# Kernel tuning notes

Measured on AMD Instinct MI355X. Metric: run time of the kernel, lower is better.

## Reference

```python
import jax, jax.numpy as jnp
import numpy as np

T, NC, NQ = 16, 32, 32
H, W, C = 128, 128, 1
DW, DR, DZ = 256, 256, 128
LABEL_DIM, Y_DIM = 2, 2
NHEADS = 8
NFEAT = int(DW * np.log(DW))  # performer default nb_features = int(d*ln d) = 1419


def setup_inputs() -> dict:
    key = jax.random.key(0)
    ks = iter(jax.random.split(key, 48))
    def nrm(shape, scale=0.02):
        return jax.random.normal(next(ks), shape, dtype=jnp.float32) * scale
    z = lambda *s: jnp.zeros(s, jnp.float32)
    return {
        'batch_train_images': jax.random.normal(next(ks), (T, NC, C, H, W), jnp.float32),
        'label_train': jax.random.normal(next(ks), (T, NC, LABEL_DIM), jnp.float32),
        'batch_test_images': jax.random.normal(next(ks), (T, NQ, C, H, W), jnp.float32),
        'conv1_w': nrm((32, C, 3, 3), 0.1), 'conv1_b': z(32),
        'conv2_w': nrm((48, 32, 3, 3), 0.05), 'conv2_b': z(48),
        'conv3_w': nrm((64, 48, 3, 3), 0.05), 'conv3_b': z(64),
        'enc_lw': nrm((DW, 4096)), 'enc_lb': z(DW),
        'ty_w': nrm((DW // 4, LABEL_DIM)), 'ty_b': z(DW // 4),
        'er_w1': nrm((DR, DW + DW // 4), 0.05), 'er_b1': z(DR),
        'er_w2': nrm((DR, DR), 0.05), 'er_b2': z(DR),
        'er_w3': nrm((DR, DR), 0.05), 'er_b3': z(DR),
        'wq': nrm((NHEADS, DW, DW), 0.05), 'wq_b': z(NHEADS, DW),
        'wk': nrm((NHEADS, DW, DW), 0.05), 'wk_b': z(NHEADS, DW),
        'wv': nrm((NHEADS, DW, DW), 0.05), 'wv_b': z(NHEADS, DW),
        'wo_w': nrm((DW, NHEADS * DW), 0.02), 'wo_b': z(DW),
        'rz_w': nrm((DZ, DR), 0.05), 'rz_b': z(DZ),
        'd0_w1': nrm((100, DW + DZ), 0.05), 'd0_b1': z(100),
        'd0_w2': nrm((100, 100), 0.05), 'd0_b2': z(100),
        'd0_w3': nrm((Y_DIM, 100), 0.05), 'd0_b3': z(Y_DIM),
        'proj': jax.random.normal(next(ks), (NFEAT, DW), jnp.float32),
    }


def _conv(x, w, b, stride):
    y = jax.lax.conv_general_dilated(x, w, (stride, stride), [(1, 1), (1, 1)],
                                     dimension_numbers=('NCHW', 'OIHW', 'NCHW'))
    return y + b[None, :, None, None]


def _maxpool2(x):
    return jax.lax.reduce_window(x, -jnp.inf, jax.lax.max, (1, 1, 2, 2), (1, 1, 2, 2), 'VALID')


def _encode(x, c1w, c1b, c2w, c2b, c3w, c3b, lw, lb):
    # BBBEncoder (mean weights): 128->64->32->pool16->8, 64ch, flatten 4096 -> DW
    x = jax.nn.relu(_conv(x, c1w, c1b, 2))
    x = jax.nn.relu(_conv(x, c2w, c2b, 2))
    x = _maxpool2(x)
    x = jax.nn.relu(_conv(x, c3w, c3b, 2))
    x = x.reshape(x.shape[0], -1)  # [B, 4096], NCHW order matches torch view
    return x @ lw.T + lb


def _softmax_kernel(x, proj, is_query):
    # performer softmax-kernel random features
    dn = x.shape[-1] ** -0.25
    ratio = proj.shape[0] ** -0.5
    xn = x * dn
    xd = jnp.einsum('bhnd,fd->bhnf', xn, proj)
    diag = 0.5 * jnp.sum(xn * xn, axis=-1, keepdims=True)
    if is_query:
        m = jnp.max(xd, axis=-1, keepdims=True)
    else:
        m = jnp.max(xd, axis=(-1, -2), keepdims=True)
    return ratio * (jnp.exp(xd - diag - jax.lax.stop_gradient(m)) + 1e-4)


def _forward(batch_train_images, label_train, batch_test_images,
             conv1_w, conv1_b, conv2_w, conv2_b, conv3_w, conv3_b, enc_lw, enc_lb,
             ty_w, ty_b, er_w1, er_b1, er_w2, er_b2, er_w3, er_b3,
             wq, wq_b, wk, wk_b, wv, wv_b, wo_w, wo_b, rz_w, rz_b,
             d0_w1, d0_b1, d0_w2, d0_b2, d0_w3, d0_b3, proj):
    enc = lambda im: _encode(im, conv1_w, conv1_b, conv2_w, conv2_b, conv3_w, conv3_b, enc_lw, enc_lb)
    x_qry = enc(batch_test_images.reshape(-1, C, H, W)).reshape(T, NQ, DW)
    x_ctx = enc(batch_train_images.reshape(-1, C, H, W)).reshape(T, NC, DW)
    ly = label_train @ ty_w.T + ty_b
    x = jnp.concatenate([x_ctx, ly], axis=2)  # [T, NC, DW + DW//4]
    h = jax.nn.relu(x @ er_w1.T + er_b1)
    h = jax.nn.relu(h @ er_w2.T + er_b2)
    rs = h @ er_w3.T + er_b3  # [T, NC, DR]
    # per-head projections (batched over the 8 heads)
    k_all = jnp.einsum('bnd,hed->bhne', x_ctx, wk) + wk_b[None, :, None, :]
    v_all = jnp.einsum('bnd,hed->bhne', rs, wv) + wv_b[None, :, None, :]
    q_all = jnp.einsum('bnd,hed->bhne', x_qry, wq) + wq_b[None, :, None, :]
    qp = _softmax_kernel(q_all, proj, True)   # [T, H, NQ, F]
    kp = _softmax_kernel(k_all, proj, False)  # [T, H, NC, F]
    d_inv = 1.0 / jnp.einsum('bhnf,bhf->bhn', qp, kp.sum(axis=2))
    ctx_mat = jnp.einsum('bhnf,bhne->bhfe', kp, v_all)
    outs = jnp.einsum('bhnf,bhfe->bhne', qp, ctx_mat) * d_inv[..., None]
    outs = outs.transpose(0, 2, 3, 1).reshape(T, NQ, -1)  # permute(0,2,3,1).view
    rep = outs @ wo_w.T + wo_b
    zz = rep @ rz_w.T + rz_b  # [T, NQ, DZ]
    xz = jnp.concatenate([x_qry, zz], axis=-1)
    h = jax.nn.relu(xz @ d0_w1.T + d0_b1)
    h = jax.nn.relu(h @ d0_w2.T + d0_b2)
    return jnp.tanh(h @ d0_w3.T + d0_b3)  # pr_y_mu [T, NQ, Y_DIM]


def reference(batch_train_images, label_train, batch_test_images,
              conv1_w, conv1_b, conv2_w, conv2_b, conv3_w, conv3_b, enc_lw, enc_lb,
              ty_w, ty_b, er_w1, er_b1, er_w2, er_b2, er_w3, er_b3,
              wq, wq_b, wk, wk_b, wv, wv_b, wo_w, wo_b, rz_w, rz_b,
              d0_w1, d0_b1, d0_w2, d0_b2, d0_w3, d0_b3, proj):
    pr_y_mu = _forward(batch_train_images, label_train, batch_test_images,
                       conv1_w, conv1_b, conv2_w, conv2_b, conv3_w, conv3_b, enc_lw, enc_lb,
                       ty_w, ty_b, er_w1, er_b1, er_w2, er_b2, er_w3, er_b3,
                       wq, wq_b, wk, wk_b, wv, wv_b, wo_w, wo_b, rz_w, rz_b,
                       d0_w1, d0_b1, d0_w2, d0_b2, d0_w3, d0_b3, proj)
    kl = jnp.float32(0.0)  # deterministic (mean-weight) BBB encoder -> KL constant
    return (pr_y_mu, kl)
```

## Files before the change

### kernel.cpp

```cpp
#include <hip/hip_runtime.h>
#include <math.h>

#define F_FEAT 1419
static constexpr float DN    = 0.25f;

typedef short short8 __attribute__((ext_vector_type(8)));
typedef float f32x4  __attribute__((ext_vector_type(4)));

static constexpr long OFF_XDQ  = 0;
static constexpr long OFF_XDK  = 5812224;
static constexpr long U_WQH = 0;
static constexpr long U_WQL = 524288;
static constexpr long U_WKH = 1048576;
static constexpr long U_WKL = 1572864;
static constexpr long U_WVH = 2097152;
static constexpr long U_WVL = 2621440;
static constexpr long OFF_ENCT = 4000000;
static constexpr long OFF_REPT = 8400000;
static constexpr long OFF_PA   = 11624448;
static constexpr long U_PH  = 23248896;
static constexpr long U_PL  = 23642112;
static constexpr long U_XCH = 24035328;
static constexpr long U_XCL = 24297472;
static constexpr long U_RSH = 24559616;
static constexpr long U_RSL = 24690688;
static constexpr long U_C3H = 25165824;
static constexpr long U_C3L = 29360128;
static constexpr long U_WOH = 25165824;
static constexpr long U_WOL = 25690112;
static constexpr long BASE     = 16777216;
static constexpr long OFF_XCTX = BASE + 0;
static constexpr long OFF_XQRY = BASE + 131072;
static constexpr long OFF_XCAT = BASE + 262144;
static constexpr long OFF_H1   = BASE + 425984;
static constexpr long OFF_H2   = BASE + 557056;
static constexpr long OFF_RS   = BASE + 688128;
static constexpr long U_QH  = (BASE + 819200) * 2;
static constexpr long U_QL  = U_QH + 1048576;
static constexpr long U_KH  = (BASE + 1867776) * 2;
static constexpr long U_KL  = U_KH + 1048576;
static constexpr long OFF_VA   = BASE + 2916352;
static constexpr long OFF_AW1  = BASE + 3964928;
static constexpr long U_ELH = (BASE + 3977344) * 2;
static constexpr long U_ELL = U_ELH + 1048576;
static constexpr long U_REPH = U_ELH;
static constexpr long U_REPL = U_ELL;
static constexpr long OFF_REP  = BASE + 5025920;
static constexpr long OFF_XZ   = BASE + 5156992;
static constexpr long OFF_DH1  = BASE + 5353600;
static constexpr long OFF_DH2  = BASE + 5404800;
static constexpr long OFF_MD   = BASE + 5456000;
static constexpr long OFF_AW   = 22233216;
static constexpr long OFF_AW3  = 22240128;

__device__ inline unsigned short f2bf(float f) {
    unsigned int x = __float_as_uint(f);
    unsigned int r = x + 0x7fffu + ((x >> 16) & 1u);
    return (unsigned short)(r >> 16);
}
__device__ inline float bf2f(unsigned short h) {
    return __uint_as_float((unsigned int)h << 16);
}
__device__ inline unsigned int cvtpk(float a, float b) {
    unsigned int r;
    asm("v_cvt_pk_bf16_f32 %0, %1, %2" : "=v"(r) : "v"(a), "v"(b));
    return r;
}
__device__ inline unsigned encf(float f) {
    unsigned u = __float_as_uint(f);
    return (u & 0x80000000u) ? ~u : (u | 0x80000000u);
}
__device__ inline float decf(unsigned u) {
    return __uint_as_float((u & 0x80000000u) ? (u & 0x7fffffffu) : ~u);
}

static constexpr int NA1 = 13824;
static constexpr int NA2 = NA1 + 1024;
static constexpr int NA3 = NA2 + 73728;
static constexpr int NA4 = NA3 + 1048576;

__global__ void k_wprepA(const float* __restrict__ w2, const float* __restrict__ w1,
                         const float* __restrict__ w3, const float* __restrict__ elw,
                         unsigned short* __restrict__ Aw, unsigned short* __restrict__ Aw1,
                         unsigned short* __restrict__ Aw3,
                         unsigned short* __restrict__ ELh, unsigned short* __restrict__ ELl)
{
    int i = blockIdx.x * 256 + threadIdx.x;
    if (i < NA1) {
        int ic  = i & 31;
        int m16 = (i >> 5) & 15;
        int emt = i >> 9;
        int mt  = emt % 3, e = emt / 3;
        Aw[i] = f2bf(w2[((mt * 16 + m16) * 32 + ic) * 9 + e]);
    } else if (i < NA2) {
        int j = i - NA1;
        int k = j & 31, m = (j >> 5) & 15, mt = j >> 9;
        Aw1[j] = (k < 9) ? f2bf(w1[(mt * 16 + m) * 9 + k]) : (unsigned short)0;
    } else if (i < NA3) {
        int j = i - NA2;
        int k  = j & 63;
        int m  = (j >> 6) & 15;
        int hl = (j >> 10) & 1;
        int mt = (j >> 11) & 3;
        int e  = j >> 13;
        unsigned short v = 0;
        if (k < 48) {
            float w = w3[((mt * 16 + m) * 48 + k) * 9 + e];
            unsigned short hi = f2bf(w);
            v = hl == 0 ? hi : f2bf(w - bf2f(hi));
        }
        Aw3[j] = v;
    } else if (i < NA4) {
        int j = i - NA3;
        float v = elw[j];
        unsigned short h = f2bf(v);
        ELh[j] = h; ELl[j] = f2bf(v - bf2f(h));
    }
}

static constexpr int NB1 = 393216;
static constexpr int NB2 = NB1 + 1572864;

__global__ void k_wprepB(const float* __restrict__ proj,
                         const float* __restrict__ wq, const float* __restrict__ wk,
                         const float* __restrict__ wv,
                         unsigned short* __restrict__ Ph, unsigned short* __restrict__ Pl,
                         unsigned short* __restrict__ Wqkv)
{
    int i = blockIdx.x * 256 + threadIdx.x;
    if (i < NB1) {
        float v = (i < 363264) ? proj[i] : 0.f;
        unsigned short h = f2bf(v);
        Ph[i] = h; Pl[i] = f2bf(v - bf2f(h));
    } else if (i < NB2) {
        int j = i - NB1;
        int y = j / 524288, jj = j % 524288;
        const float* s = (y == 0) ? wq : (y == 1) ? wk : wv;
        float v = s[jj];
        unsigned short h = f2bf(v);
        Wqkv[(long)y * 1048576 + jj] = h;
        Wqkv[(long)y * 1048576 + 524288 + jj] = f2bf(v - bf2f(h));
    }
}

#define TP 136
__launch_bounds__(256)
__global__ void k_conv12m(const float* __restrict__ train, const float* __restrict__ test,
                          const float* __restrict__ b1,
                          const unsigned short* __restrict__ Aw,
                          const unsigned short* __restrict__ Aw1,
                          const float* __restrict__ b2,
                          unsigned short* __restrict__ pool_out)
{
    const int g   = blockIdx.x;
    const int img = blockIdx.y;
    const float* in = (img < 512) ? (train + (long)img * 16384)
                                  : (test  + (long)(img - 512) * 16384);

    __shared__ unsigned short ring[9 * 66 * 40];
    __shared__ unsigned short tile[19 * TP];

    const int t = threadIdx.x;

    for (int i = t; i < 9 * 40; i += 256) {
        int sl = i / 40, icp = i % 40;
        ring[(sl * 66 + 0) * 40 + icp] = 0;
    }
    if (g == 0)
        for (int i = t; i < 66 * 40; i += 256) ring[i] = 0;
    if (t < 19) *(unsigned int*)&tile[t * TP + 2] = 0u;

    {
        const float4 z4 = make_float4(0.f, 0.f, 0.f, 0.f);
        for (int u = t; u < 19 * 32; u += 256) {
            int row = u >> 5, k = u & 31;
            int r2 = 16 * g - 3 + row;
            float4 v = (r2 >= 0) ? *(const float4*)(in + r2 * 128 + k * 4) : z4;
            uint2 d;
            d.x = cvtpk(v.x, v.y);
            d.y = cvtpk(v.z, v.w);
            *(uint2*)&tile[row * TP + 4 + k * 4] = d;
        }
    }
    __syncthreads();

    const int w    = t >> 6;
    const int lane = t & 63;
    const int cn   = lane & 15;
    const int quad = lane >> 4;

    short8 a1f0 = *(const short8*)&Aw1[(0 * 16 + cn) * 32 + quad * 8];
    short8 a1f1 = *(const short8*)&Aw1[(16 + cn) * 32 + quad * 8];
    float4 bsa = *(const float4*)&b1[quad * 4];
    float4 bsb = *(const float4*)&b1[16 + quad * 4];

    const int px2 = w * 16 + cn;
    const int tb  = 2 * px2 + 2;
    auto do_slice = [&](int sl) {
        const int rb = 2 * sl * TP + tb;
        uint4 pk = make_uint4(0u, 0u, 0u, 0u);
        if (quad == 0) {
            unsigned int w00 = *(const unsigned int*)&tile[rb];
            unsigned int w10 = *(const unsigned int*)&tile[rb + 2];
            unsigned int w01 = *(const unsigned int*)&tile[rb + TP];
            unsigned int w11 = *(const unsigned int*)&tile[rb + TP + 2];
            unsigned int w02 = *(const unsigned int*)&tile[rb + 2 * TP];
            unsigned int w12 = *(const unsigned int*)&tile[rb + 2 * TP + 2];
            pk.x = (w00 >> 16) | (w10 << 16);
            pk.y = (w10 >> 16) | (w01 & 0xffff0000u);
            pk.z = w11;
            pk.w = (w02 >> 16) | (w12 << 16);
        } else if (quad == 1) {
            pk.x = (*(const unsigned int*)&tile[rb + 2 * TP + 2]) >> 16;
        }
        short8 bfr = *(const short8*)&pk;
        f32x4 z = (f32x4){0.f, 0.f, 0.f, 0.f};
        f32x4 c0 = __builtin_amdgcn_mfma_f32_16x16x32_bf16(a1f0, bfr, z, 0, 0, 0);
        f32x4 c1 = __builtin_amdgcn_mfma_f32_16x16x32_bf16(a1f1, bfr, z, 0, 0, 0);
        uint2 u0, u1;
        u0.x = cvtpk(fmaxf(c0[0] + bsa.x, 0.f), fmaxf(c0[1] + bsa.y, 0.f));
        u0.y = cvtpk(fmaxf(c0[2] + bsa.z, 0.f), fmaxf(c0[3] + bsa.w, 0.f));
        u1.x = cvtpk(fmaxf(c1[0] + bsb.x, 0.f), fmaxf(c1[1] + bsb.y, 0.f));
        u1.y = cvtpk(fmaxf(c1[2] + bsb.z, 0.f), fmaxf(c1[3] + bsb.w, 0.f));
        *(uint2*)&ring[(sl * 66 + px2 + 1) * 40 + quad * 4]      = u0;
        *(uint2*)&ring[(sl * 66 + px2 + 1) * 40 + 16 + quad * 4] = u1;
    };
    if (g > 0) do_slice(0);
    #pragma unroll
    for (int sl = 1; sl < 9; sl++) do_slice(sl);

    short8 ca0 = *(const short8*)&Aw[((0 * 3 + 0) * 16 + cn) * 32 + quad * 8];
    short8 ca1 = *(const short8*)&Aw[((0 * 3 + 1) * 16 + cn) * 32 + quad * 8];
    short8 ca2 = *(const short8*)&Aw[((0 * 3 + 2) * 16 + cn) * 32 + quad * 8];
    __syncthreads();

    const int pr = w >> 1, xh = w & 1;
    f32x4 acc[3][2];
    #pragma unroll
    for (int mt = 0; mt < 3; mt++) {
        acc[mt][0] = (f32x4){0.f, 0.f, 0.f, 0.f};
        acc[mt][1] = (f32x4){0.f, 0.f, 0.f, 0.f};
    }

    #pragma unroll
    for (int e = 0; e < 9; e++) {
        int dy = e / 3, dx = e - 3 * dy;
        int c  = 2 * (xh * 16 + cn) + dx;
        int s0 = 4 * pr + dy;
        short8 b0  = *(const short8*)&ring[(s0 * 66 + c) * 40 + quad * 8];
        short8 b1f = *(const short8*)&ring[((s0 + 2) * 66 + c) * 40 + quad * 8];
        short8 na0, na1, na2;
        if (e < 8) {
            na0 = *(const short8*)&Aw[(((e + 1) * 3 + 0) * 16 + cn) * 32 + quad * 8];
            na1 = *(const short8*)&Aw[(((e + 1) * 3 + 1) * 16 + cn) * 32 + quad * 8];
            na2 = *(const short8*)&Aw[(((e + 1) * 3 + 2) * 16 + cn) * 32 + quad * 8];
        }
        acc[0][0] = __builtin_amdgcn_mfma_f32_16x16x32_bf16(ca0, b0,  acc[0][0], 0, 0, 0);
        acc[1][0] = __builtin_amdgcn_mfma_f32_16x16x32_bf16(ca1, b0,  acc[1][0], 0, 0, 0);
        acc[2][0] = __builtin_amdgcn_mfma_f32_16x16x32_bf16(ca2, b0,  acc[2][0], 0, 0, 0);
        acc[0][1] = __builtin_amdgcn_mfma_f32_16x16x32_bf16(ca0, b1f, acc[0][1], 0, 0, 0);
        acc[1][1] = __builtin_amdgcn_mfma_f32_16x16x32_bf16(ca1, b1f, acc[1][1], 0, 0, 0);
        acc[2][1] = __builtin_amdgcn_mfma_f32_16x16x32_bf16(ca2, b1f, acc[2][1], 0, 0, 0);
        if (e < 8) { ca0 = na0; ca1 = na1; ca2 = na2; }
    }

    {
        const int prow = 2 * g + pr;
        const int ppx  = xh * 8 + (cn >> 1);
        unsigned short* pb = pool_out + ((long)img * 256 + prow * 16 + ppx) * 96
                           + ((cn & 1) ? 48 : 0);
        #pragma unroll
        for (int mt = 0; mt < 3; mt++) {
            float4 bv = *(const float4*)&b2[mt * 16 + quad * 4];
            float m0, m1, m2, m3;
            {
                float v;
                v = fmaxf(fmaxf(acc[mt][0][0] + bv.x, acc[mt][1][0] + bv.x), 0.f);
                m0 = fmaxf(v, __shfl_xor(v, 1));
                v = fmaxf(fmaxf(acc[mt][0][1] + bv.y, acc[mt][1][1] + bv.y), 0.f);
                m1 = fmaxf(v, __shfl_xor(v, 1));
                v = fmaxf(fmaxf(acc[mt][0][2] + bv.z, acc[mt][1][2] + bv.z), 0.f);
                m2 = fmaxf(v, __shfl_xor(v, 1));
                v = fmaxf(fmaxf(acc[mt][0][3] + bv.w, acc[mt][1][3] + bv.w), 0.f);
                m3 = fmaxf(v, __shfl_xor(v, 1));
            }
            uint2 hv;
            hv.x = cvtpk(m0, m1);
            hv.y = cvtpk(m2, m3);
            uint2 sv = hv;
            if (cn & 1) {
                float d0 = m0 - bf2f((unsigned short)(hv.x & 0xffffu));
                float d1 = m1 - bf2f((unsigned short)(hv.x >> 16));
                float d2 = m2 - bf2f((unsigned short)(hv.y & 0xffffu));
                float d3 = m3 - bf2f((unsigned short)(hv.y >> 16));
                sv.x = cvtpk(d0, d1);
                sv.y = cvtpk(d2, d3);
            }
            *(uint2*)&pb[mt * 16 + quad * 4] = sv;
        }
    }
}

#define C3PITCH 104
__launch_bounds__(512)
__global__ void k_conv3m(const unsigned short* __restrict__ pool,
                         const unsigned short* __restrict__ Aw3,
                         const float* __restrict__ b3,
                         unsigned short* __restrict__ C3h, unsigned short* __restrict__ C3l)
{
    const int img = blockIdx.x;
    __shared__ unsigned short s_in[30120];
    const int t = threadIdx.x;

    uint4* s4 = (uint4*)s_in;
    const uint4 zz = make_uint4(0, 0, 0, 0);
    for (int i = t; i < 3765; i += 512) s4[i] = zz;
    __syncthreads();
    {
        int p = t >> 1, half = t & 1;
        const uint4* src = (const uint4*)(pool + ((long)img * 256 + p) * 96 + half * 48);
        int r = p >> 4, c = p & 15;
        uint4* dst = (uint4*)(s_in + ((r + 1) * 17 + (c + 1)) * C3PITCH + half * 48);
        #pragma unroll
        for (int j = 0; j < 6; j++) dst[j] = src[j];
    }
    __syncthreads();

    const int w = t >> 6, lane = t & 63;
    const int n = lane & 15, quad = lane >> 4;
    const int mt = w >> 1, ntb = (w & 1) * 2;

    f32x4 acc[2];
    acc[0] = (f32x4){0.f, 0.f, 0.f, 0.f};
    acc[1] = (f32x4){0.f, 0.f, 0.f, 0.f};

    for (int e = 0; e < 9; e++) {
        int dy = e / 3, dx = e - 3 * dy;
        const unsigned short* A0 = Aw3 + (long)(((e * 4 + mt) * 2 + 0) * 16 + n) * 64 + quad * 8;
        const unsigned short* A1 = Aw3 + (long)(((e * 4 + mt) * 2 + 1) * 16 + n) * 64 + quad * 8;
        short8 ah0 = *(const short8*)(A0);
        short8 ah1 = *(const short8*)(A0 + 32);
        short8 al0 = *(const short8*)(A1);
        short8 al1 = *(const short8*)(A1 + 32);
        #pragma unroll
        for (int j = 0; j < 2; j++) {
            int p = (ntb + j) * 16 + n;
            int y = p >> 3, x = p & 7;
            const unsigned short* Bp = s_in + ((2 * y + dy) * 17 + (2 * x + dx)) * C3PITCH + quad * 8;
            short8 bh0 = *(const short8*)(Bp);
            short8 bh1 = *(const short8*)(Bp + 32);
            short8 bl0 = *(const short8*)(Bp + 48);
            short8 bl1 = *(const short8*)(Bp + 48 + 32);
            acc[j] = __builtin_amdgcn_mfma_f32_16x16x32_bf16(ah0, bh0, acc[j], 0, 0, 0);
// ... 92 lines not shown
                    (Yf + (long)z * sY)[(long)row * ldY + col] = v;
                } else if (OUTMODE == 0) {
                    if (B) v += B[col];
                    (Yf + (long)z * sY)[(long)row * ldY + col] = v;
                } else {
                    if (B) v += B[col];
                    unsigned short h = f2bf(v);
                    (Yh + (long)z * sY)[(long)row * ldY + col] = h;
                    (Yl + (long)z * sY)[(long)row * ldY + col] = f2bf(v - bf2f(h));
                }
            }
        }
    }
}

__launch_bounds__(256)
__global__ void mgemm128(const unsigned short* __restrict__ Xh0, const unsigned short* __restrict__ Xl0,
                         const unsigned short* __restrict__ Wh, const unsigned short* __restrict__ Wl,
                         float* __restrict__ Yf, int M, int N, int K, int ldY, float scale,
                         long sX, long sY,
                         unsigned* __restrict__ mqe, unsigned* __restrict__ mke)
{
    const int z = blockIdx.z;
    const unsigned short* Xh = Xh0 + (long)z * sX;
    const unsigned short* Xl = Xl0 + (long)z * sX;

    __shared__ unsigned short sAh[128 * 40], sAl[128 * 40], sBh[128 * 40], sBl[128 * 40];

    const int t = threadIdx.x;
    const int m0 = blockIdx.y * 128, n0 = blockIdx.x * 128;
    const int r = t >> 1, kq = (t & 1) * 16;

    const int w = t >> 6, lane = t & 63;
    const int wm = (w & 1) * 64, wn = (w >> 1) * 64;
    const int cn = lane & 15, quad = lane >> 4;

    f32x4 acc[4][4];
    #pragma unroll
    for (int i = 0; i < 4; i++)
        #pragma unroll
        for (int j = 0; j < 4; j++) acc[i][j] = (f32x4){0.f, 0.f, 0.f, 0.f};

    for (int kb = 0; kb < K; kb += 32) {
        *(uint4*)&sAh[r * 40 + kq]     = *(const uint4*)&Xh[(long)(m0 + r) * K + kb + kq];
        *(uint4*)&sAh[r * 40 + kq + 8] = *(const uint4*)&Xh[(long)(m0 + r) * K + kb + kq + 8];
        *(uint4*)&sAl[r * 40 + kq]     = *(const uint4*)&Xl[(long)(m0 + r) * K + kb + kq];
        *(uint4*)&sAl[r * 40 + kq + 8] = *(const uint4*)&Xl[(long)(m0 + r) * K + kb + kq + 8];
        *(uint4*)&sBh[r * 40 + kq]     = *(const uint4*)&Wh[(long)(n0 + r) * K + kb + kq];
        *(uint4*)&sBh[r * 40 + kq + 8] = *(const uint4*)&Wh[(long)(n0 + r) * K + kb + kq + 8];
        *(uint4*)&sBl[r * 40 + kq]     = *(const uint4*)&Wl[(long)(n0 + r) * K + kb + kq];
        *(uint4*)&sBl[r * 40 + kq + 8] = *(const uint4*)&Wl[(long)(n0 + r) * K + kb + kq + 8];
        __syncthreads();
        short8 axh[4], axl[4], bxh[4], bxl[4];
        #pragma unroll
        for (int i = 0; i < 4; i++) {
            axh[i] = *(const short8*)&sAh[(wm + i * 16 + cn) * 40 + quad * 8];
            axl[i] = *(const short8*)&sAl[(wm + i * 16 + cn) * 40 + quad * 8];
            bxh[i] = *(const short8*)&sBh[(wn + i * 16 + cn) * 40 + quad * 8];
            bxl[i] = *(const short8*)&sBl[(wn + i * 16 + cn) * 40 + quad * 8];
        }
        #pragma unroll
        for (int i = 0; i < 4; i++)
            #pragma unroll
            for (int j = 0; j < 4; j++) {
                acc[i][j] = __builtin_amdgcn_mfma_f32_16x16x32_bf16(axh[i], bxh[j], acc[i][j], 0, 0, 0);
                acc[i][j] = __builtin_amdgcn_mfma_f32_16x16x32_bf16(axh[i], bxl[j], acc[i][j], 0, 0, 0);
                acc[i][j] = __builtin_amdgcn_mfma_f32_16x16x32_bf16(axl[i], bxh[j], acc[i][j], 0, 0, 0);
            }
        __syncthreads();
    }

    float gmax0 = -3e38f, gmax1 = -3e38f;
    #pragma unroll
    for (int i = 0; i < 4; i++) {
        #pragma unroll
        for (int reg = 0; reg < 4; reg++) {
            int row = m0 + wm + i * 16 + quad * 4 + reg;
            float rmax = -3e38f;
            #pragma unroll
            for (int j = 0; j < 4; j++) {
                int col = n0 + wn + j * 16 + cn;
                if (col >= N) continue;
                float v = acc[i][j][reg] * scale;
                (Yf + (long)z * sY)[(long)row * ldY + col] = v;
                rmax = fmaxf(rmax, v);
            }
            if (z == 0) {
                rmax = fmaxf(rmax, __shfl_xor(rmax, 1));
                rmax = fmaxf(rmax, __shfl_xor(rmax, 2));
                rmax = fmaxf(rmax, __shfl_xor(rmax, 4));
                rmax = fmaxf(rmax, __shfl_xor(rmax, 8));
                if (cn == 0) atomicMax(&mqe[row], encf(rmax));
            } else {
                if (i < 2) gmax0 = fmaxf(gmax0, rmax);
                else       gmax1 = fmaxf(gmax1, rmax);
            }
        }
    }
    if (z == 1) {
        for (int d = 1; d < 64; d <<= 1) {
            gmax0 = fmaxf(gmax0, __shfl_xor(gmax0, d));
            gmax1 = fmaxf(gmax1, __shfl_xor(gmax1, d));
        }
        if (lane == 0) {
            atomicMax(&mke[(m0 + wm) >> 5],       encf(gmax0));
            atomicMax(&mke[((m0 + wm) >> 5) + 1], encf(gmax1));
        }
    }
}

__launch_bounds__(256)
__global__ void mgemm128s(const unsigned short* __restrict__ Xh, const unsigned short* __restrict__ Xl,
                          const unsigned short* __restrict__ Wh, const unsigned short* __restrict__ Wl,
                          float* __restrict__ Yf, int M, int N, int K, int ldY,
                          long sY, int kChunk)
{
    const int z = blockIdx.z;
    const int k0 = z * kChunk, k1 = min(K, k0 + kChunk);

    __shared__ unsigned short sAh[128 * 40], sAl[128 * 40], sBh[128 * 40], sBl[128 * 40];

    const int t = threadIdx.x;
    const int m0 = blockIdx.y * 128, n0 = blockIdx.x * 128;
    const int r = t >> 1, kq = (t & 1) * 16;

    const int w = t >> 6, lane = t & 63;
    const int wm = (w & 1) * 64, wn = (w >> 1) * 64;
    const int cn = lane & 15, quad = lane >> 4;

    f32x4 acc[4][4];
    #pragma unroll
    for (int i = 0; i < 4; i++)
        #pragma unroll
        for (int j = 0; j < 4; j++) acc[i][j] = (f32x4){0.f, 0.f, 0.f, 0.f};

    for (int kb = k0; kb < k1; kb += 32) {
        *(uint4*)&sAh[r * 40 + kq]     = *(const uint4*)&Xh[(long)(m0 + r) * K + kb + kq];
        *(uint4*)&sAh[r * 40 + kq + 8] = *(const uint4*)&Xh[(long)(m0 + r) * K + kb + kq + 8];
        *(uint4*)&sAl[r * 40 + kq]     = *(const uint4*)&Xl[(long)(m0 + r) * K + kb + kq];
        *(uint4*)&sAl[r * 40 + kq + 8] = *(const uint4*)&Xl[(long)(m0 + r) * K + kb + kq + 8];
        *(uint4*)&sBh[r * 40 + kq]     = *(const uint4*)&Wh[(long)(n0 + r) * K + kb + kq];
        *(uint4*)&sBh[r * 40 + kq + 8] = *(const uint4*)&Wh[(long)(n0 + r) * K + kb + kq + 8];
        *(uint4*)&sBl[r * 40 + kq]     = *(const uint4*)&Wl[(long)(n0 + r) * K + kb + kq];
        *(uint4*)&sBl[r * 40 + kq + 8] = *(const uint4*)&Wl[(long)(n0 + r) * K + kb + kq + 8];
        __syncthreads();
        short8 axh[4], axl[4], bxh[4], bxl[4];
        #pragma unroll
        for (int i = 0; i < 4; i++) {
            axh[i] = *(const short8*)&sAh[(wm + i * 16 + cn) * 40 + quad * 8];
            axl[i] = *(const short8*)&sAl[(wm + i * 16 + cn) * 40 + quad * 8];
            bxh[i] = *(const short8*)&sBh[(wn + i * 16 + cn) * 40 + quad * 8];
            bxl[i] = *(const short8*)&sBl[(wn + i * 16 + cn) * 40 + quad * 8];
        }
        #pragma unroll
        for (int i = 0; i < 4; i++)
            #pragma unroll
            for (int j = 0; j < 4; j++) {
                acc[i][j] = __builtin_amdgcn_mfma_f32_16x16x32_bf16(axh[i], bxh[j], acc[i][j], 0, 0, 0);
                acc[i][j] = __builtin_amdgcn_mfma_f32_16x16x32_bf16(axh[i], bxl[j], acc[i][j], 0, 0, 0);
                acc[i][j] = __builtin_amdgcn_mfma_f32_16x16x32_bf16(axl[i], bxh[j], acc[i][j], 0, 0, 0);
            }
        __syncthreads();
    }

    float* Y = Yf + (long)z * sY;
    #pragma unroll
    for (int i = 0; i < 4; i++) {
        #pragma unroll
        for (int reg = 0; reg < 4; reg++) {
            int row = m0 + wm + i * 16 + quad * 4 + reg;
            #pragma unroll
            for (int j = 0; j < 4; j++) {
                int col = n0 + wn + j * 16 + cn;
                if (col >= N) continue;
                Y[(long)row * ldY + col] = acc[i][j][reg];
            }
        }
    }
}

__launch_bounds__(256)
__global__ void k_qkv(const unsigned short* __restrict__ XCh, const unsigned short* __restrict__ XCl,
                      const unsigned short* __restrict__ RSh, const unsigned short* __restrict__ RSl,
                      const unsigned short* __restrict__ Wqkv,
                      const float* __restrict__ wqb, const float* __restrict__ wkb,
                      const float* __restrict__ wvb,
                      unsigned short* __restrict__ Qh, unsigned short* __restrict__ Ql,
                      unsigned short* __restrict__ Kh, unsigned short* __restrict__ Kl,
                      float* __restrict__ v_all, float* __restrict__ dq, float* __restrict__ dk)
{
    const int z = blockIdx.z, y = z >> 3, zh = z & 7;
    const unsigned short* Xh = (y == 0) ? XCh + 512 * 256 : (y == 1) ? XCh : RSh;
    const unsigned short* Xl = (y == 0) ? XCl + 512 * 256 : (y == 1) ? XCl : RSl;
    const unsigned short* Wh = Wqkv + (long)y * 1048576 + (long)zh * 65536;
    const unsigned short* Wl = Wh + 524288;
    const float* B = ((y == 0) ? wqb : (y == 1) ? wkb : wvb) + zh * 256;

    __shared__ unsigned short sAh[64 * 40], sAl[64 * 40], sBh[64 * 40], sBl[64 * 40];

    const int t = threadIdx.x;
    const int m0 = blockIdx.y * 64, n0 = blockIdx.x * 64;
    const int r = t >> 2, kq = (t & 3) * 8;
    const int w = t >> 6, lane = t & 63;
    const int wm = (w & 1) * 32, wn = (w >> 1) * 32;
    const int cn = lane & 15, quad = lane >> 4;

    f32x4 acc[2][2];
    acc[0][0] = acc[0][1] = acc[1][0] = acc[1][1] = (f32x4){0.f, 0.f, 0.f, 0.f};

    for (int kb = 0; kb < 256; kb += 32) {
        *(uint4*)&sAh[r * 40 + kq] = *(const uint4*)&Xh[(long)(m0 + r) * 256 + kb + kq];
        *(uint4*)&sAl[r * 40 + kq] = *(const uint4*)&Xl[(long)(m0 + r) * 256 + kb + kq];
        *(uint4*)&sBh[r * 40 + kq] = *(const uint4*)&Wh[(long)(n0 + r) * 256 + kb + kq];
        *(uint4*)&sBl[r * 40 + kq] = *(const uint4*)&Wl[(long)(n0 + r) * 256 + kb + kq];
        __syncthreads();
        short8 axh[2], axl[2], bxh[2], bxl[2];
        #pragma unroll
        for (int i = 0; i < 2; i++) {
            axh[i] = *(const short8*)&sAh[(wm + i * 16 + cn) * 40 + quad * 8];
            axl[i] = *(const short8*)&sAl[(wm + i * 16 + cn) * 40 + quad * 8];
            bxh[i] = *(const short8*)&sBh[(wn + i * 16 + cn) * 40 + quad * 8];
            bxl[i] = *(const short8*)&sBl[(wn + i * 16 + cn) * 40 + quad * 8];
        }
        #pragma unroll
        for (int i = 0; i < 2; i++)
            #pragma unroll
            for (int j = 0; j < 2; j++) {
                acc[i][j] = __builtin_amdgcn_mfma_f32_16x16x32_bf16(axh[i], bxh[j], acc[i][j], 0, 0, 0);
                acc[i][j] = __builtin_amdgcn_mfma_f32_16x16x32_bf16(axh[i], bxl[j], acc[i][j], 0, 0, 0);
                acc[i][j] = __builtin_amdgcn_mfma_f32_16x16x32_bf16(axl[i], bxh[j], acc[i][j], 0, 0, 0);
            }
        __syncthreads();
    }

    unsigned short* Yh = ((y == 0) ? Qh : Kh) + (long)zh * 131072;
    unsigned short* Yl = ((y == 0) ? Ql : Kl) + (long)zh * 131072;
    float* Yf = v_all + (long)zh * 131072;
    float* dacc = ((y == 0) ? dq : dk) + zh * 512;

    #pragma unroll
    for (int i = 0; i < 2; i++) {
        #pragma unroll
        for (int reg = 0; reg < 4; reg++) {
            int row = m0 + wm + i * 16 + quad * 4 + reg;
            float s = 0.f;
            #pragma unroll
            for (int j = 0; j < 2; j++) {
                int col = n0 + wn + j * 16 + cn;
                float v = acc[i][j][reg] + B[col];
                if (y == 2) {
                    Yf[(long)row * 256 + col] = v;
                } else {
                    unsigned short h = f2bf(v);
                    Yh[(long)row * 256 + col] = h;
                    Yl[(long)row * 256 + col] = f2bf(v - bf2f(h));
                    s += v * v;
                }
            }
            if (y < 2) {
                s += __shfl_xor(s, 1); s += __shfl_xor(s, 2);
                s += __shfl_xor(s, 4); s += __shfl_xor(s, 8);
                if (cn == 0) atomicAdd(&dacc[row], s * (1.f / 32.f));
            }
        }
    }
}

__global__ void k_red_enc(const float* __restrict__ tmp, const float* __restrict__ elb,
                          float* __restrict__ x_ctx, unsigned short* __restrict__ XCh,
                          unsigned short* __restrict__ XCl, float* __restrict__ xcat,
                          const float* __restrict__ label, const float* __restrict__ tyw,
                          const float* __restrict__ tyb,
                          const float* __restrict__ wow, unsigned short* __restrict__ WOh,
                          unsigned short* __restrict__ WOl, unsigned* __restrict__ md)
{
    int b = blockIdx.x;
    int tt = threadIdx.x;
    if (b < 1024) {
        int i = b * 256 + tt;
        int r = i >> 8, c = i & 255;
        float v = elb[c];
        #pragma unroll
        for (int z = 0; z < 16; z++) v += tmp[(long)z * 262144 + i];
        x_ctx[i] = v;
        unsigned short h = f2bf(v);
        XCh[i] = h; XCl[i] = f2bf(v - bf2f(h));
        if (r < 512) xcat[r * 320 + c] = v;
    } else if (b < 1152) {
        int i = (b - 1024) * 256 + tt;
        int r = i >> 6, e = i & 63;
        xcat[r * 320 + 256 + e] = tyb[e] + label[r * 2] * tyw[e * 2] + label[r * 2 + 1] * tyw[e * 2 + 1];
    } else if (b < 3200) {
        int i = (b - 1152) * 256 + tt;
        float v = wow[i];
        unsigned short h = f2bf(v);
        WOh[i] = h; WOl[i] = f2bf(v - bf2f(h));
    } else {
        int i = (b - 3200) * 256 + tt;
        if (i < 12416) md[i] = 0u;
    }
}

__global__ void k_red_rep(const float* __restrict__ tmp, const float* __restrict__ wob,
                          float* __restrict__ rep,
                          const float* __restrict__ xq, float* __restrict__ xz)
{
    int b = blockIdx.x;
    int tt = threadIdx.x;
    if (b < 512) {
        int i = b * 256 + tt;
        int c = i & 255;
        float v = wob[c];
        #pragma unroll
        for (int z = 0; z < 8; z++) v += tmp[(long)z * 131072 + i];
        rep[i] = v;
    } else {
        int i = (b - 512) * 256 + tt;
        int r = i >> 8, c = i & 255;
        xz[r * 384 + c] = xq[i];
    }
}

template<int BM, int BN, int BK, int ACT, bool FIN, bool WP>
__launch_bounds__(256)
__global__ void gemm_k(const float* __restrict__ X, const float* __restrict__ W,
                       const float* __restrict__ B, float* __restrict__ Y,
                       int M, int N, int K, int ldY,
                       unsigned short* __restrict__ Ph2, unsigned short* __restrict__ Pl2)
{
    __shared__ float As[BK][BM + 4];
    __shared__ float Bs[BK][BN + 4];
    const int t = threadIdx.x;
    const int tx = t & 15, ty = t >> 4;
    const int m0 = blockIdx.y * BM, n0 = blockIdx.x * BN;
    float acc[2][2] = {{0.f, 0.f}, {0.f, 0.f}};

    for (int kb = 0; kb < K; kb += BK) {
        for (int i = t; i < BM * BK; i += 256) {
            int rr = i / BK, c = i % BK;
            int mm = m0 + rr, kk = kb + c;
            As[c][rr] = (mm < M && kk < K) ? X[(long)mm * K + kk] : 0.f;
        }
        for (int i = t; i < BN * BK; i += 256) {
            int rr = i / BK, c = i % BK;
            int nn = n0 + rr, kk = kb + c;
            Bs[c][rr] = (nn < N && kk < K) ? W[(long)nn * K + kk] : 0.f;
        }
        __syncthreads();
        #pragma unroll
        for (int kk = 0; kk < BK; kk++) {
            float2 a2 = *(const float2*)&As[kk][ty * 2];
            float2 b2 = *(const float2*)&Bs[kk][tx * 2];
            acc[0][0] += a2.x * b2.x; acc[0][1] += a2.x * b2.y;
            acc[1][0] += a2.y * b2.x; acc[1][1] += a2.y * b2.y;
        }
        __syncthreads();
    }

    #pragma unroll
    for (int i = 0; i < 2; i++) {
        int mm = m0 + ty * 2 + i;
        if (mm >= M) continue;
        #pragma unroll
        for (int j = 0; j < 2; j++) {
            int nn = n0 + tx * 2 + j;
            if (nn >= N) continue;
            float v = acc[i][j] + (B ? B[nn] : 0.f);
            if (ACT == 1) v = fmaxf(v, 0.f);
            if (ACT == 2) v = tanhf(v);
            Y[(long)mm * ldY + nn] = v;
            if (WP) {
                unsigned short h = f2bf(v);
                Ph2[(long)mm * ldY + nn] = h;
                Pl2[(long)mm * ldY + nn] = f2bf(v - bf2f(h));
            }
        }
    }
    if (FIN && t == 0 && blockIdx.x == 0 && blockIdx.y == 0) Y[1024] = 0.f;
}

#define NSPLIT 4
#define FCH 355
__launch_bounds__(256)
__global__ void k_attn1(const float* __restrict__ qp, const float* __restrict__ kp,
                        const float* __restrict__ dq, const unsigned* __restrict__ mqe,
                        const float* __restrict__ dk, const unsigned* __restrict__ mke,
                        float* __restrict__ pA)
{
    const int s  = blockIdx.x;
    const int kb = blockIdx.y;
    const long row0 = (long)kb * 32;
    const int f0 = s * FCH;
    const int f1 = min(F_FEAT, f0 + FCH);

    __shared__ float s_q[32 * 65];
    __shared__ float s_k[32 * 65];
    __shared__ float s_cq[32], s_ck[32];

    const int t = threadIdx.x;
    const int n = t >> 3;
    const int mq_ = (t & 7) * 4;

    if (t < 32) {
        s_cq[t] = dq[row0 + t] + decf(mqe[row0 + t]);
        s_ck[t] = dk[row0 + t] + decf(mke[kb]);
    }
    __syncthreads();

    float acc[4] = {0.f, 0.f, 0.f, 0.f};
    for (int fc = f0; fc < f1; fc += 64) {
        for (int i = t; i < 2048; i += 256) {
            int rr = i >> 6, ff = i & 63;
            int fg = fc + ff;
            float qv = 0.f, kv = 0.f;
            if (fg < f1) {
                qv = __expf(qp[(row0 + rr) * F_FEAT + fg] - s_cq[rr]) + 1e-4f;
                kv = __expf(kp[(row0 + rr) * F_FEAT + fg] - s_ck[rr]) + 1e-4f;
            }
            s_q[rr * 65 + ff] = qv;
            s_k[rr * 65 + ff] = kv;
        }
        __syncthreads();
        #pragma unroll 8
        for (int ff = 0; ff < 64; ff++) {
            float a = s_q[n * 65 + ff];
            #pragma unroll
            for (int j = 0; j < 4; j++) acc[j] += a * s_k[(mq_ + j) * 65 + ff];
        }
        __syncthreads();
    }

    float* dst = pA + ((long)kb * NSPLIT + s) * 1024;
    #pragma unroll
    for (int j = 0; j < 4; j++) dst[n * 32 + mq_ + j] = acc[j];
}

__launch_bounds__(256)
__global__ void k_attn2(const float* __restrict__ pA, const float* __restrict__ va,
                        unsigned short* __restrict__ REPh, unsigned short* __restrict__ REPl)
{
    const int ec = blockIdx.x;
    const int kb = blockIdx.y;
    const int h = kb >> 4, tt = kb & 15;
    const long row0 = (long)kb * 32;

    __shared__ float s_A[32][33];
    __shared__ float s_di[32];
    __shared__ float s_v[32 * 64];

    const int t = threadIdx.x;

    {
        const float* base = pA + (long)kb * NSPLIT * 1024 + t * 4;
        float4 v0 = *(const float4*)(base);
        float4 v1 = *(const float4*)(base + 1024);
        float4 v2 = *(const float4*)(base + 2048);
        float4 v3 = *(const float4*)(base + 3072);
        int r = t >> 3, c = (t & 7) * 4;
        s_A[r][c]     = v0.x + v1.x + v2.x + v3.x;
        s_A[r][c + 1] = v0.y + v1.y + v2.y + v3.y;
        s_A[r][c + 2] = v0.z + v1.z + v2.z + v3.z;
        s_A[r][c + 3] = v0.w + v1.w + v2.w + v3.w;
    }
    for (int i = t; i < 2048; i += 256) {
        int m = i >> 6, e = i & 63;
        s_v[m * 64 + e] = va[row0 * 256 + m * 256 + ec * 64 + e];
    }
    __syncthreads();
    if (t < 32) {
        float s = 0.f;
        #pragma unroll
        for (int m = 0; m < 32; m++) s += s_A[t][m];
        s_di[t] = 1.f / s;
    }
    __syncthreads();

    const int n = t >> 3, e0 = t & 7;
    float out[8];
    #pragma unroll
    for (int j = 0; j < 8; j++) out[j] = 0.f;
    for (int m = 0; m < 32; m++) {
        float a = s_A[n][m];
        #pragma unroll
        for (int j = 0; j < 8; j++) out[j] += a * s_v[m * 64 + e0 + 8 * j];
    }
    float di = s_di[n];
    unsigned short* dsth = REPh + ((long)tt * 32 + n) * 2048;
    unsigned short* dstl = REPl + ((long)tt * 32 + n) * 2048;
    #pragma unroll
    for (int j = 0; j < 8; j++) {
        int e = ec * 64 + e0 + 8 * j;
        float val = out[j] * di;
        unsigned short hh = f2bf(val);
        dsth[e * 8 + h] = hh;
        dstl[e * 8 + h] = f2bf(val - bf2f(hh));
    }
}

extern "C" void kernel_launch(void* const* d_in, const int* in_sizes, int n_in,
                              void* d_out, int out_size, void* d_ws, size_t ws_size,
                              hipStream_t stream)
{
    const float* train  = (const float*)d_in[0];
    const float* label  = (const float*)d_in[1];
    const float* test   = (const float*)d_in[2];
    const float* c1w = (const float*)d_in[3];  const float* c1b = (const float*)d_in[4];
    const float* c2w = (const float*)d_in[5];  const float* c2b = (const float*)d_in[6];
    const float* c3w = (const float*)d_in[7];  const float* c3b = (const float*)d_in[8];
    const float* elw = (const float*)d_in[9];  const float* elb = (const float*)d_in[10];
    const float* tyw = (const float*)d_in[11]; const float* tyb = (const float*)d_in[12];
    const float* ew1 = (const float*)d_in[13]; const float* eb1 = (const float*)d_in[14];
    const float* ew2 = (const float*)d_in[15]; const float* eb2 = (const float*)d_in[16];
    const float* ew3 = (const float*)d_in[17]; const float* eb3 = (const float*)d_in[18];
    const float* wq  = (const float*)d_in[19]; const float* wqb = (const float*)d_in[20];
    const float* wk  = (const float*)d_in[21]; const float* wkb = (const float*)d_in[22];
    const float* wv  = (const float*)d_in[23]; const float* wvb = (const float*)d_in[24];
    const float* wow = (const float*)d_in[25]; const float* wob = (const float*)d_in[26];
    const float* rzw = (const float*)d_in[27]; const float* rzb = (const float*)d_in[28];
    const float* dw1 = (const float*)d_in[29]; const float* db1 = (const float*)d_in[30];
    const float* dw2 = (const float*)d_in[31]; const float* db2 = (const float*)d_in[32];
    const float* dw3 = (const float*)d_in[33]; const float* db3 = (const float*)d_in[34];
    const float* proj= (const float*)d_in[35];

    float* wsf = (float*)d_ws;
    unsigned short* usw = (unsigned short*)d_ws;
    float* out = (float*)d_out;

    unsigned short* A_pool = usw;
    float* x_ctx  = wsf + OFF_XCTX;
    float* x_qry  = wsf + OFF_XQRY;
    float* xcat   = wsf + OFF_XCAT;
    float* h1     = wsf + OFF_H1;
    float* h2     = wsf + OFF_H2;
    float* rs     = wsf + OFF_RS;
    float* v_all  = wsf + OFF_VA;
    float* rep    = wsf + OFF_REP;
    float* xz     = wsf + OFF_XZ;
    float* dh1    = wsf + OFF_DH1;
    float* dh2    = wsf + OFF_DH2;
    float* xd_q   = wsf + OFF_XDQ;
    float* xd_k   = wsf + OFF_XDK;
    float* enc_t  = wsf + OFF_ENCT;
    float* rep_t  = wsf + OFF_REPT;
    float* pA     = wsf + OFF_PA;
    float* dqv    = wsf + OFF_MD;
    unsigned* mqe = (unsigned*)(wsf + OFF_MD + 4096);
    float* dkv    = wsf + OFF_MD + 8192;
    unsigned* mke = (unsigned*)(wsf + OFF_MD + 12288);
    unsigned* mdw = (unsigned*)(wsf + OFF_MD);
    unsigned short* Aw  = (unsigned short*)(wsf + OFF_AW);
    unsigned short* Aw3 = (unsigned short*)(wsf + OFF_AW3);
    unsigned short* Aw1 = (unsigned short*)(wsf + OFF_AW1);

    unsigned short* Wqkv = usw + U_WQH;
    unsigned short* Ph  = usw + U_PH;  unsigned short* Pl  = usw + U_PL;
    unsigned short* XCh = usw + U_XCH; unsigned short* XCl = usw + U_XCL;
    unsigned short* RSh = usw + U_RSH; unsigned short* RSl = usw + U_RSL;
    unsigned short* C3h = usw + U_C3H; unsigned short* C3l = usw + U_C3L;
    unsigned short* Qh  = usw + U_QH;  unsigned short* Ql  = usw + U_QL;
    unsigned short* Kh  = usw + U_KH;  unsigned short* Kl  = usw + U_KL;
    unsigned short* ELh = usw + U_ELH; unsigned short* ELl = usw + U_ELL;
    unsigned short* WOh = usw + U_WOH; unsigned short* WOl = usw + U_WOL;
    unsigned short* REPh= usw + U_REPH;unsigned short* REPl= usw + U_REPL;

    k_wprepA<<<4442, 256, 0, stream>>>(c2w, c1w, c3w, elw, Aw, Aw1, Aw3, ELh, ELl);

    k_conv12m<<<dim3(8, 1024), 256, 0, stream>>>(train, test, c1b, Aw, Aw1, c2b, A_pool);
    k_conv3m<<<1024, 512, 0, stream>>>(A_pool, Aw3, c3b, C3h, C3l);

    k_wprepB<<<7680, 256, 0, stream>>>(proj, wq, wk, wv, Ph, Pl, Wqkv);

    mgemm128s<<<dim3(2, 8, 16), 256, 0, stream>>>(
        C3h, C3l, ELh, ELl, enc_t, 1024, 256, 4096, 256, 262144, 256);
    k_red_enc<<<3249, 256, 0, stream>>>(enc_t, elb, x_ctx, XCh, XCl, xcat,
                                        label, tyw, tyb, wow, WOh, WOl, mdw);

    gemm_k<32,32,32,1,false,false><<<dim3(8, 16), 256, 0, stream>>>(xcat, ew1, eb1, h1, 512, 256, 320, 256, nullptr, nullptr);
    gemm_k<32,32,32,1,false,false><<<dim3(8, 16), 256, 0, stream>>>(h1, ew2, eb2, h2, 512, 256, 256, 256, nullptr, nullptr);
    gemm_k<32,32,32,0,false,true ><<<dim3(8, 16), 256, 0, stream>>>(h2, ew3, eb3, rs, 512, 256, 256, 256, RSh, RSl);

    k_qkv<<<dim3(4, 8, 24), 256, 0, stream>>>(XCh, XCl, RSh, RSl, Wqkv,
                                              wqb, wkb, wvb, Qh, Ql, Kh, Kl,
                                              v_all, dqv, dkv);

    mgemm128<<<dim3(12, 32, 2), 256, 0, stream>>>(
        Qh, Ql, Ph, Pl, xd_q,
        4096, F_FEAT, 256, F_FEAT, DN, 2097152, 5812224, mqe, mke);

    k_attn1<<<dim3(NSPLIT, 128), 256, 0, stream>>>(xd_q, xd_k, dqv, mqe, dkv, mke, pA);
    k_attn2<<<dim3(4, 128), 256, 0, stream>>>(pA, v_all, REPh, REPl);

    mgemm<3><<<dim3(4, 8, 8), 256, 0, stream>>>(
        REPh, REPl, WOh, WOl, nullptr, rep_t, nullptr, nullptr,
        512, 256, 2048, 256, 1.f, 0, 0, 0, 131072, 256);
    k_red_rep<<<1024, 256, 0, stream>>>(rep_t, wob, rep, x_qry, xz);

    gemm_k<32,32,32,0,false,false><<<dim3(4, 16), 256, 0, stream>>>(rep, rzw, rzb, xz + 256, 512, 128, 256, 384, nullptr, nullptr);

    gemm_k<32,32,32,1,false,false><<<dim3(4, 16), 256, 0, stream>>>(xz, dw1, db1, dh1, 512, 100, 384, 100, nullptr, nullptr);
    gemm_k<32,32,32,1,false,false><<<dim3(4, 16), 256, 0, stream>>>(dh1, dw2, db2, dh2, 512, 100, 100, 100, nullptr, nullptr);
    gemm_k<32,32,32,2,true ,false><<<dim3(1, 16), 256, 0, stream>>>(dh2, dw3, db3, out, 512, 2, 100, 2, nullptr, nullptr);
}
```

Baseline: 633.9 us.

## Fuse encoder-residual MLP and decoder MLP chains into single row-block kernels

Replaces the three-launch encoder residual MLP with one kernel that keeps 8 rows per block in shared memory through all three layers and writes only the bf16 hi/lo split outputs. Likewise fuses the rz projection, concat and three decoder layers into one kernel, removing the xz concat copy and the intermediate global buffers. This cuts six kernel launches and their global round trips. In exchange, only 64 blocks run and each thread streams weight rows from global with no register tiling, so per-block weight traffic and low occupancy may be costly.

```diff
diff --git a/kernel.cpp b/kernel.cpp
--- a/kernel.cpp
+++ b/kernel.cpp
@@ -32,9 +32,6 @@
 static constexpr long OFF_XCTX = BASE + 0;
 static constexpr long OFF_XQRY = BASE + 131072;
 static constexpr long OFF_XCAT = BASE + 262144;
-static constexpr long OFF_H1   = BASE + 425984;
-static constexpr long OFF_H2   = BASE + 557056;
-static constexpr long OFF_RS   = BASE + 688128;
 static constexpr long U_QH  = (BASE + 819200) * 2;
 static constexpr long U_QL  = U_QH + 1048576;
 static constexpr long U_KH  = (BASE + 1867776) * 2;
@@ -46,9 +43,6 @@
 static constexpr long U_REPH = U_ELH;
 static constexpr long U_REPL = U_ELL;
 static constexpr long OFF_REP  = BASE + 5025920;
-static constexpr long OFF_XZ   = BASE + 5156992;
-static constexpr long OFF_DH1  = BASE + 5353600;
-static constexpr long OFF_DH2  = BASE + 5404800;
 static constexpr long OFF_MD   = BASE + 5456000;
 static constexpr long OFF_AW   = 22233216;
 static constexpr long OFF_AW3  = 22240128;
@@ -747,81 +741,153 @@
 }
 
 __global__ void k_red_rep(const float* __restrict__ tmp, const float* __restrict__ wob,
-                          float* __restrict__ rep,
-                          const float* __restrict__ xq, float* __restrict__ xz)
-{
-    int b = blockIdx.x;
-    int tt = threadIdx.x;
-    if (b < 512) {
-        int i = b * 256 + tt;
-        int c = i & 255;
-        float v = wob[c];
-        #pragma unroll
-        for (int z = 0; z < 8; z++) v += tmp[(long)z * 131072 + i];
-        rep[i] = v;
-    } else {
-        int i = (b - 512) * 256 + tt;
-        int r = i >> 8, c = i & 255;
-        xz[r * 384 + c] = xq[i];
-    }
-}
-
-template<int BM, int BN, int BK, int ACT, bool FIN, bool WP>
+                          float* __restrict__ rep)
+{
+    int i = blockIdx.x * 256 + threadIdx.x;
+    int c = i & 255;
+    float v = wob[c];
+    #pragma unroll
+    for (int z = 0; z < 8; z++) v += tmp[(long)z * 131072 + i];
+    rep[i] = v;
+}
+
 __launch_bounds__(256)
-__global__ void gemm_k(const float* __restrict__ X, const float* __restrict__ W,
-                       const float* __restrict__ B, float* __restrict__ Y,
-                       int M, int N, int K, int ldY,
-                       unsigned short* __restrict__ Ph2, unsigned short* __restrict__ Pl2)
-{
-    __shared__ float As[BK][BM + 4];
-    __shared__ float Bs[BK][BN + 4];
+__global__ void k_ermlp(const float* __restrict__ xcat,
+                        const float* __restrict__ ew1, const float* __restrict__ eb1,
+                        const float* __restrict__ ew2, const float* __restrict__ eb2,
+                        const float* __restrict__ ew3, const float* __restrict__ eb3,
+                        unsigned short* __restrict__ RSh, unsigned short* __restrict__ RSl)
+{
+    __shared__ float s_x[8 * 320];
+    __shared__ float s_h[8 * 256];
+    __shared__ float s_h2[8 * 256];
     const int t = threadIdx.x;
-    const int tx = t & 15, ty = t >> 4;
-    const int m0 = blockIdx.y * BM, n0 = blockIdx.x * BN;
-    float acc[2][2] = {{0.f, 0.f}, {0.f, 0.f}};
-
-    for (int kb = 0; kb < K; kb += BK) {
-        for (int i = t; i < BM * BK; i += 256) {
-            int rr = i / BK, c = i % BK;
-            int mm = m0 + rr, kk = kb + c;
-            As[c][rr] = (mm < M && kk < K) ? X[(long)mm * K + kk] : 0.f;
-        }
-        for (int i = t; i < BN * BK; i += 256) {
-            int rr = i / BK, c = i % BK;
-            int nn = n0 + rr, kk = kb + c;
-            Bs[c][rr] = (nn < N && kk < K) ? W[(long)nn * K + kk] : 0.f;
-        }
-        __syncthreads();
-        #pragma unroll
-        for (int kk = 0; kk < BK; kk++) {
-            float2 a2 = *(const float2*)&As[kk][ty * 2];
-            float2 b2 = *(const float2*)&Bs[kk][tx * 2];
-            acc[0][0] += a2.x * b2.x; acc[0][1] += a2.x * b2.y;
-            acc[1][0] += a2.y * b2.x; acc[1][1] += a2.y * b2.y;
-        }
-        __syncthreads();
-    }
-
-    #pragma unroll
-    for (int i = 0; i < 2; i++) {
-        int mm = m0 + ty * 2 + i;
-        if (mm >= M) continue;
-        #pragma unroll
-        for (int j = 0; j < 2; j++) {
-            int nn = n0 + tx * 2 + j;
-            if (nn >= N) continue;
-            float v = acc[i][j] + (B ? B[nn] : 0.f);
-            if (ACT == 1) v = fmaxf(v, 0.f);
-            if (ACT == 2) v = tanhf(v);
-            Y[(long)mm * ldY + nn] = v;
-            if (WP) {
-                unsigned short h = f2bf(v);
-                Ph2[(long)mm * ldY + nn] = h;
-                Pl2[(long)mm * ldY + nn] = f2bf(v - bf2f(h));
-            }
-        }
-    }
-    if (FIN && t == 0 && blockIdx.x == 0 && blockIdx.y == 0) Y[1024] = 0.f;
+    const int row0 = blockIdx.x * 8;
+    const int rg = t >> 5, lane = t & 31;
+
+    for (int i = t; i < 8 * 320; i += 256) s_x[i] = xcat[(long)row0 * 320 + i];
+    __syncthreads();
+
+    for (int col = lane; col < 256; col += 32) {
+        float acc = eb1[col];
+        const float* w = ew1 + (long)col * 320;
+        const float* x = s_x + rg * 320;
+        for (int k = 0; k < 320; k += 4) {
+            float4 wv = *(const float4*)(w + k);
+            float4 xv = *(const float4*)(x + k);
+            acc += xv.x * wv.x; acc += xv.y * wv.y; acc += xv.z * wv.z; acc += xv.w * wv.w;
+        }
+        s_h[rg * 256 + col] = fmaxf(acc, 0.f);
+    }
+    __syncthreads();
+    for (int col = lane; col < 256; col += 32) {
+        float acc = eb2[col];
+        const float* w = ew2 + (long)col * 256;
+        const float* x = s_h + rg * 256;
+        for (int k = 0; k < 256; k += 4) {
+            float4 wv = *(const float4*)(w + k);
+            float4 xv = *(const float4*)(x + k);
+            acc += xv.x * wv.x; acc += xv.y * wv.y; acc += xv.z * wv.z; acc += xv.w * wv.w;
+        }
+        s_h2[rg * 256 + col] = fmaxf(acc, 0.f);
+    }
+    __syncthreads();
+    for (int col = lane; col < 256; col += 32) {
+        float acc = eb3[col];
+        const float* w = ew3 + (long)col * 256;
+        const float* x = s_h2 + rg * 256;
+        for (int k = 0; k < 256; k += 4) {
+            float4 wv = *(const float4*)(w + k);
+            float4 xv = *(const float4*)(x + k);
+            acc += xv.x * wv.x; acc += xv.y * wv.y; acc += xv.z * wv.z; acc += xv.w * wv.w;
+        }
+        unsigned short h = f2bf(acc);
+        RSh[(long)(row0 + rg) * 256 + col] = h;
+        RSl[(long)(row0 + rg) * 256 + col] = f2bf(acc - bf2f(h));
+    }
+}
+
+__launch_bounds__(256)
+__global__ void k_dec(const float* __restrict__ xq, const float* __restrict__ rep,
+                      const float* __restrict__ rzw, const float* __restrict__ rzb,
+                      const float* __restrict__ dw1, const float* __restrict__ db1,
+                      const float* __restrict__ dw2, const float* __restrict__ db2,
+                      const float* __restrict__ dw3, const float* __restrict__ db3,
+                      float* __restrict__ out)
+{
+    __shared__ float s_xq[8 * 256];
+    __shared__ float s_rep[8 * 256];
+    __shared__ float s_zz[8 * 128];
+    __shared__ float s_h1[8 * 104];
+    __shared__ float s_h2[8 * 104];
+    const int t = threadIdx.x;
+    const int row0 = blockIdx.x * 8;
+    const int rg = t >> 5, lane = t & 31;
+
+    for (int i = t; i < 8 * 256; i += 256) {
+        s_xq[i]  = xq[(long)row0 * 256 + i];
+        s_rep[i] = rep[(long)row0 * 256 + i];
+    }
+    __syncthreads();
+
+    for (int col = lane; col < 128; col += 32) {
+        float acc = rzb[col];
+        const float* w = rzw + (long)col * 256;
+        const float* x = s_rep + rg * 256;
+        for (int k = 0; k < 256; k += 4) {
+            float4 wv = *(const float4*)(w + k);
+            float4 xv = *(const float4*)(x + k);
+            acc += xv.x * wv.x; acc += xv.y * wv.y; acc += xv.z * wv.z; acc += xv.w * wv.w;
+        }
+        s_zz[rg * 128 + col] = acc;
+    }
+    __syncthreads();
+
+    for (int col = lane; col < 100; col += 32) {
+        float acc = db1[col];
+        const float* w = dw1 + (long)col * 384;
+        const float* x = s_xq + rg * 256;
+        for (int k = 0; k < 256; k += 4) {
+            float4 wv = *(const float4*)(w + k);
+            float4 xv = *(const float4*)(x + k);
+            acc += xv.x * wv.x; acc += xv.y * wv.y; acc += xv.z * wv.z; acc += xv.w * wv.w;
+        }
+        const float* w2 = w + 256;
+        const float* z = s_zz + rg * 128;
+        for (int k = 0; k < 128; k += 4) {
+            float4 wv = *(const float4*)(w2 + k);
+            float4 xv = *(const float4*)(z + k);
+            acc += xv.x * wv.x; acc += xv.y * wv.y; acc += xv.z * wv.z; acc += xv.w * wv.w;
+        }
+        s_h1[rg * 104 + col] = fmaxf(acc, 0.f);
+    }
+    __syncthreads();
+
+    for (int col = lane; col < 100; col += 32) {
+        float acc = db2[col];
+        const float* w = dw2 + (long)col * 100;
+        const float* x = s_h1 + rg * 104;
+        for (int k = 0; k < 100; k += 4) {
+            float4 wv = *(const float4*)(w + k);
+            float4 xv = *(const float4*)(x + k);
+            acc += xv.x * wv.x; acc += xv.y * wv.y; acc += xv.z * wv.z; acc += xv.w * wv.w;
+        }
+        s_h2[rg * 104 + col] = fmaxf(acc, 0.f);
+    }
+    __syncthreads();
+
+    if (lane < 2) {
+        float acc = db3[lane];
+        const float* w = dw3 + (long)lane * 100;
+        const float* x = s_h2 + rg * 104;
+        for (int k = 0; k < 100; k += 4) {
+            float4 wv = *(const float4*)(w + k);
+            float4 xv = *(const float4*)(x + k);
+            acc += xv.x * wv.x; acc += xv.y * wv.y; acc += xv.z * wv.z; acc += xv.w * wv.w;
+        }
+        out[(long)(row0 + rg) * 2 + lane] = tanhf(acc);
+    }
+    if (blockIdx.x == 0 && t == 0) out[1024] = 0.f;
 }
 
 #define NSPLIT 4
@@ -975,14 +1041,8 @@
     float* x_ctx  = wsf + OFF_XCTX;
     float* x_qry  = wsf + OFF_XQRY;
     float* xcat   = wsf + OFF_XCAT;
-    float* h1     = wsf + OFF_H1;
-    float* h2     = wsf + OFF_H2;
-    float* rs     = wsf + OFF_RS;
     float* v_all  = wsf + OFF_VA;
     float* rep    = wsf + OFF_REP;
-    float* xz     = wsf + OFF_XZ;
-    float* dh1    = wsf + OFF_DH1;
-    float* dh2    = wsf + OFF_DH2;
     float* xd_q   = wsf + OFF_XDQ;
     float* xd_k   = wsf + OFF_XDK;
     float* enc_t  = wsf + OFF_ENCT;
@@ -1020,9 +1080,7 @@
     k_red_enc<<<3249, 256, 0, stream>>>(enc_t, elb, x_ctx, XCh, XCl, xcat,
                                         label, tyw, tyb, wow, WOh, WOl, mdw);
 
-    gemm_k<32,32,32,1,false,false><<<dim3(8, 16), 256, 0, stream>>>(xcat, ew1, eb1, h1, 512, 256, 320, 256, nullptr, nullptr);
-    gemm_k<32,32,32,1,false,false><<<dim3(8, 16), 256, 0, stream>>>(h1, ew2, eb2, h2, 512, 256, 256, 256, nullptr, nullptr);
-    gemm_k<32,32,32,0,false,true ><<<dim3(8, 16), 256, 0, stream>>>(h2, ew3, eb3, rs, 512, 256, 256, 256, RSh, RSl);
+    k_ermlp<<<64, 256, 0, stream>>>(xcat, ew1, eb1, ew2, eb2, ew3, eb3, RSh, RSl);
 
     k_qkv<<<dim3(4, 8, 24), 256, 0, stream>>>(XCh, XCl, RSh, RSl, Wqkv,
                                               wqb, wkb, wvb, Qh, Ql, Kh, Kl,
@@ -1038,11 +1096,8 @@
     mgemm<3><<<dim3(4, 8, 8), 256, 0, stream>>>(
         REPh, REPl, WOh, WOl, nullptr, rep_t, nullptr, nullptr,
         512, 256, 2048, 256, 1.f, 0, 0, 0, 131072, 256);
-    k_red_rep<<<1024, 256, 0, stream>>>(rep_t, wob, rep, x_qry, xz);
-
-    gemm_k<32,32,32,0,false,false><<<dim3(4, 16), 256, 0, stream>>>(rep, rzw, rzb, xz + 256, 512, 128, 256, 384, nullptr, nullptr);
-
-    gemm_k<32,32,32,1,false,false><<<dim3(4, 16), 256, 0, stream>>>(xz, dw1, db1, dh1, 512, 100, 384, 100, nullptr, nullptr);
-    gemm_k<32,32,32,1,false,false><<<dim3(4, 16), 256, 0, stream>>>(dh1, dw2, db2, dh2, 512, 100, 100, 100, nullptr, nullptr);
-    gemm_k<32,32,32,2,true ,false><<<dim3(1, 16), 256, 0, stream>>>(dh2, dw3, db3, out, 512, 2, 100, 2, nullptr, nullptr);
-}
+    k_red_rep<<<512, 256, 0, stream>>>(rep_t, wob, rep);
+
+    k_dec<<<64, 256, 0, stream>>>(x_qry, rep, rzw, rzb, dw1, db1, dw2, db2,
+                                  dw3, db3, out);
+}
```

New measurement: 781.2 us. +23.2%, slower.
